# Kernel optimization log

Measured on AMD Instinct MI355X. Metric: run time of the kernel, lower is better.

## Reference

```python
import jax, jax.numpy as jnp
import numpy as np
from jax.scipy.special import logsumexp

N_ALPHA = 8192
N_BETA = 8192
N_LAYERS = 16


def setup_inputs() -> dict:
    key = jax.random.key(0)
    k1, k2, k3 = jax.random.split(key, 3)
    alpha = jax.random.uniform(k1, (N_ALPHA,), jnp.float32, 1e-3, 1.0)
    alpha = alpha / alpha.sum()
    beta = jax.random.uniform(k2, (N_BETA,), jnp.float32, 1e-3, 1.0)
    beta = beta / beta.sum()
    C = jax.random.uniform(k3, (N_ALPHA, N_BETA), jnp.float32, 0.0, 1.0)
    eps = jnp.float32(0.1)
    return {"alpha": alpha, "beta": beta, "C": C, "eps": eps}


def reference(alpha, beta, C, eps):
    # Log-domain Sinkhorn iterations (tol=None -> run all n_layers).
    log_alpha = jnp.log(alpha)
    log_beta = jnp.log(beta)

    def step(carry, _):
        _, g = carry
        # log_dot_exp(C, g, eps): logsumexp over n_beta axis of (-C + g[None,:]) / eps
        f = eps * (log_alpha - logsumexp((g[None, :] - C) / eps, axis=-1))
        # log_dot_exp(C.T, f, eps): logsumexp over n_alpha axis of (-C + f[:,None]) / eps
        g_new = eps * (log_beta - logsumexp((f[:, None] - C) / eps, axis=0))
        return (f, g_new), None

    init = (jnp.zeros_like(alpha), jnp.zeros_like(beta))
    (f, g), _ = jax.lax.scan(step, init, None, length=N_LAYERS)
    return f, g
```

## Files before the change

kernel.cpp:

```cpp
#include <hip/hip_runtime.h>

#define NA 8192
#define NB 8192
#define N_LAYERS 16
#define ROWS_PER_RC 128
#define N_RC (NA / ROWS_PER_RC)

typedef _Float16 half_t;
typedef _Float16 half4_t __attribute__((ext_vector_type(4)));
typedef _Float16 half8_t __attribute__((ext_vector_type(8)));
typedef float float4_t __attribute__((ext_vector_type(4)));

template <bool WRITE_E>
__global__ __launch_bounds__(256) void sink_u_first(
    const float* __restrict__ C, const float* __restrict__ alpha,
    const float* __restrict__ d_eps, half_t* __restrict__ E,
    float* __restrict__ u)
{
    const int row = blockIdx.x;
    const int t = threadIdx.x;
    const float inv_eps = 1.0f / d_eps[0];
    const float4_t* Crow = (const float4_t*)(C + (size_t)row * NB);
    half4_t* Erow = (half4_t*)(E + (size_t)row * NB);

    float s = 0.0f;
#pragma unroll
    for (int k = 0; k < 8; ++k) {
        const int idx = k * 256 + t;
        float4_t c = Crow[idx];
        float e0 = __expf(-c.x * inv_eps);
        float e1 = __expf(-c.y * inv_eps);
        float e2 = __expf(-c.z * inv_eps);
        float e3 = __expf(-c.w * inv_eps);
        if (WRITE_E) {
            half4_t h;
            h.x = (_Float16)e0; h.y = (_Float16)e1;
            h.z = (_Float16)e2; h.w = (_Float16)e3;
            Erow[idx] = h;
        }
        s += (e0 + e1) + (e2 + e3);
    }

    __shared__ float sm[256];
    sm[t] = s;
    __syncthreads();
    for (int off = 128; off > 0; off >>= 1) {
        if (t < off) sm[t] += sm[t + off];
        __syncthreads();
    }
    if (t == 0) u[row] = alpha[row] / sm[0];
}

template <bool USE_E>
__global__ __launch_bounds__(256) void sink_u_step(
    const void* __restrict__ mat, const float* __restrict__ v,
    const float* __restrict__ alpha, const float* __restrict__ d_eps,
    float* __restrict__ u)
{
    const int row = blockIdx.x;
    const int t = threadIdx.x;
    const float4_t* vv = (const float4_t*)v;
    float s = 0.0f;

    if (USE_E) {
        const half4_t* Erow = (const half4_t*)mat + (size_t)row * (NB / 4);
#pragma unroll
        for (int k = 0; k < 8; ++k) {
            const int idx = k * 256 + t;
            half4_t e = Erow[idx];
            float4_t w = vv[idx];
            s += (float)e.x * w.x + (float)e.y * w.y +
                 (float)e.z * w.z + (float)e.w * w.w;
        }
    } else {
        const float inv_eps = 1.0f / d_eps[0];
        const float4_t* Crow = (const float4_t*)mat + (size_t)row * (NB / 4);
#pragma unroll
        for (int k = 0; k < 8; ++k) {
            const int idx = k * 256 + t;
            float4_t c = Crow[idx];
            float4_t w = vv[idx];
            s += __expf(-c.x * inv_eps) * w.x + __expf(-c.y * inv_eps) * w.y +
                 __expf(-c.z * inv_eps) * w.z + __expf(-c.w * inv_eps) * w.w;
        }
    }

    __shared__ float sm[256];
    sm[t] = s;
    __syncthreads();
    for (int off = 128; off > 0; off >>= 1) {
        if (t < off) sm[t] += sm[t + off];
        __syncthreads();
    }
    if (t == 0) u[row] = alpha[row] / sm[0];
}

template <bool USE_E>
__global__ __launch_bounds__(256) void sink_v_partial(
    const void* __restrict__ mat, const float* __restrict__ u,
    const float* __restrict__ d_eps, float* __restrict__ partial)
{
    const int cc = blockIdx.x;
    const int rc = blockIdx.y;
    const int t = threadIdx.x;
    const int row0 = rc * ROWS_PER_RC;

    float acc[8];
#pragma unroll
    for (int k = 0; k < 8; ++k) acc[k] = 0.0f;

    if (USE_E) {
        const half8_t* Eb = (const half8_t*)mat;
        const int g = cc * 256 + t;
#pragma unroll 4
        for (int r = 0; r < ROWS_PER_RC; ++r) {
            const float ur = u[row0 + r];
            half8_t e = Eb[(size_t)(row0 + r) * (NB / 8) + g];
#pragma unroll
            for (int k = 0; k < 8; ++k) acc[k] += ur * (float)e[k];
        }
    } else {
        const float inv_eps = 1.0f / d_eps[0];
        const float4_t* Cb = (const float4_t*)mat;
        const int g = (cc * 256 + t) * 2;
#pragma unroll 2
        for (int r = 0; r < ROWS_PER_RC; ++r) {
            const float ur = u[row0 + r];
            float4_t c0 = Cb[(size_t)(row0 + r) * (NB / 4) + g];
            float4_t c1 = Cb[(size_t)(row0 + r) * (NB / 4) + g + 1];
            acc[0] += ur * __expf(-c0.x * inv_eps);
            acc[1] += ur * __expf(-c0.y * inv_eps);
            acc[2] += ur * __expf(-c0.z * inv_eps);
            acc[3] += ur * __expf(-c0.w * inv_eps);
            acc[4] += ur * __expf(-c1.x * inv_eps);
            acc[5] += ur * __expf(-c1.y * inv_eps);
            acc[6] += ur * __expf(-c1.z * inv_eps);
            acc[7] += ur * __expf(-c1.w * inv_eps);
        }
    }

    float4_t o0 = {acc[0], acc[1], acc[2], acc[3]};
    float4_t o1 = {acc[4], acc[5], acc[6], acc[7]};
    float4_t* p = (float4_t*)(partial + (size_t)rc * NB + (size_t)(cc * 256 + t) * 8);
    p[0] = o0;
    p[1] = o1;
}

__global__ __launch_bounds__(256) void sink_v_combine(
    const float* __restrict__ partial, const float* __restrict__ beta,
    float* __restrict__ v)
{
    const int col = blockIdx.x * 256 + threadIdx.x;
    float s = 0.0f;
#pragma unroll 8
    for (int rc = 0; rc < N_RC; ++rc) s += partial[(size_t)rc * NB + col];
    v[col] = beta[col] / s;
}

__global__ __launch_bounds__(256) void sink_finalize(
    const float* __restrict__ u, const float* __restrict__ v,
    const float* __restrict__ d_eps, float* __restrict__ out)
{
    const int i = blockIdx.x * 256 + threadIdx.x;
    const float eps = d_eps[0];
    if (i < NA) {
        out[i] = eps * logf(u[i]);
    } else if (i < NA + NB) {
        out[i] = eps * logf(v[i - NA]);
    }
}

extern "C" void kernel_launch(void* const* d_in, const int* in_sizes, int n_in,
                              void* d_out, int out_size, void* d_ws, size_t ws_size,
                              hipStream_t stream)
{
    const float* alpha = (const float*)d_in[0];
    const float* beta  = (const float*)d_in[1];
    const float* C     = (const float*)d_in[2];
    const float* d_eps = (const float*)d_in[3];
    float* out = (float*)d_out;

    const size_t eBytes = (size_t)NA * NB * sizeof(half_t);
    const size_t pBytes = (size_t)N_RC * NB * sizeof(float);
    const size_t vecBytes = (size_t)NA * sizeof(float);

    char* ws = (char*)d_ws;
    const bool useE = ws_size >= eBytes + pBytes + 2 * vecBytes;

    size_t off = 0;
    half_t* E = nullptr;
    if (useE) { E = (half_t*)ws; off += eBytes; }
    float* partial = (float*)(ws + off); off += pBytes;
    float* u = (float*)(ws + off); off += vecBytes;
    float* v = (float*)(ws + off); off += vecBytes;

    const dim3 blk(256);
    const dim3 gridRow(NA);
    const dim3 gridVP(NB / 2048, N_RC);
    const dim3 gridVC(NB / 256);

    for (int layer = 0; layer < N_LAYERS; ++layer) {
        if (layer == 0) {
            if (useE)
                sink_u_first<true><<<gridRow, blk, 0, stream>>>(C, alpha, d_eps, E, u);
            else
                sink_u_first<false><<<gridRow, blk, 0, stream>>>(C, alpha, d_eps, nullptr, u);
        } else {
            if (useE)
                sink_u_step<true><<<gridRow, blk, 0, stream>>>(E, v, alpha, d_eps, u);
            else
                sink_u_step<false><<<gridRow, blk, 0, stream>>>(C, v, alpha, d_eps, u);
        }
        if (useE)
            sink_v_partial<true><<<gridVP, blk, 0, stream>>>(E, u, d_eps, partial);
        else
            sink_v_partial<false><<<gridVP, blk, 0, stream>>>(C, u, d_eps, partial);
        sink_v_combine<<<gridVC, blk, 0, stream>>>(partial, beta, v);
    }
    sink_finalize<<<dim3((NA + NB) / 256), blk, 0, stream>>>(u, v, d_eps, out);
}
```

Measured before the change: 1.201 ms.

## Fuse column combine into atomic accumulation and use wave-per-row u step

Removes the separate combine kernel and the partial-sums buffer. The column partials are atomically added into a double-buffered column-sum vector, which the u-step kernel zeroes for the next layer. The u step now computes v on the fly as beta * rcp(s) and assigns one wave per row, reducing with shuffles instead of shared memory. This saves one launch per layer and the partial traffic, at the cost of 8192*128 float atomics per layer, nondeterministic summation order, and approximate reciprocals.

```diff
diff --git a/kernel.cpp b/kernel.cpp
--- a/kernel.cpp
+++ b/kernel.cpp
@@ -3,8 +3,8 @@
 #define NA 8192
 #define NB 8192
 #define N_LAYERS 16
-#define ROWS_PER_RC 128
-#define N_RC (NA / ROWS_PER_RC)
+#define ROWS_PER_VC 64
+#define N_VC (NA / ROWS_PER_VC)
 
 typedef _Float16 half_t;
 typedef _Float16 half4_t __attribute__((ext_vector_type(4)));
@@ -15,7 +15,7 @@
 __global__ __launch_bounds__(256) void sink_u_first(
     const float* __restrict__ C, const float* __restrict__ alpha,
     const float* __restrict__ d_eps, half_t* __restrict__ E,
-    float* __restrict__ u)
+    float* __restrict__ u, float* __restrict__ s_next)
 {
     const int row = blockIdx.x;
     const int t = threadIdx.x;
@@ -48,62 +48,78 @@
         if (t < off) sm[t] += sm[t + off];
         __syncthreads();
     }
-    if (t == 0) u[row] = alpha[row] / sm[0];
+    if (t == 0) {
+        u[row] = alpha[row] / sm[0];
+        s_next[row] = 0.0f;
+    }
 }
 
 template <bool USE_E>
 __global__ __launch_bounds__(256) void sink_u_step(
-    const void* __restrict__ mat, const float* __restrict__ v,
-    const float* __restrict__ alpha, const float* __restrict__ d_eps,
-    float* __restrict__ u)
-{
-    const int row = blockIdx.x;
-    const int t = threadIdx.x;
-    const float4_t* vv = (const float4_t*)v;
-    float s = 0.0f;
+    const void* __restrict__ mat, const float* __restrict__ s_prev,
+    const float* __restrict__ beta, const float* __restrict__ alpha,
+    const float* __restrict__ d_eps, float* __restrict__ u,
+    float* __restrict__ s_next)
+{
+    const int wave = threadIdx.x >> 6;
+    const int lane = threadIdx.x & 63;
+    const int row = blockIdx.x * 4 + wave;
+
+    const float4_t* bb = (const float4_t*)beta;
+    const float4_t* ss = (const float4_t*)s_prev;
+    float acc = 0.0f;
 
     if (USE_E) {
-        const half4_t* Erow = (const half4_t*)mat + (size_t)row * (NB / 4);
-#pragma unroll
-        for (int k = 0; k < 8; ++k) {
-            const int idx = k * 256 + t;
-            half4_t e = Erow[idx];
-            float4_t w = vv[idx];
-            s += (float)e.x * w.x + (float)e.y * w.y +
-                 (float)e.z * w.z + (float)e.w * w.w;
+        const half8_t* Erow = (const half8_t*)mat + (size_t)row * (NB / 8);
+#pragma unroll 4
+        for (int k = 0; k < 16; ++k) {
+            const int g = k * 64 + lane;
+            half8_t e = Erow[g];
+            float4_t b0 = bb[2 * g],     b1 = bb[2 * g + 1];
+            float4_t s0 = ss[2 * g],     s1 = ss[2 * g + 1];
+            acc += (float)e[0] * (b0.x * __builtin_amdgcn_rcpf(s0.x));
+            acc += (float)e[1] * (b0.y * __builtin_amdgcn_rcpf(s0.y));
+            acc += (float)e[2] * (b0.z * __builtin_amdgcn_rcpf(s0.z));
+            acc += (float)e[3] * (b0.w * __builtin_amdgcn_rcpf(s0.w));
+            acc += (float)e[4] * (b1.x * __builtin_amdgcn_rcpf(s1.x));
+            acc += (float)e[5] * (b1.y * __builtin_amdgcn_rcpf(s1.y));
+            acc += (float)e[6] * (b1.z * __builtin_amdgcn_rcpf(s1.z));
+            acc += (float)e[7] * (b1.w * __builtin_amdgcn_rcpf(s1.w));
         }
     } else {
         const float inv_eps = 1.0f / d_eps[0];
         const float4_t* Crow = (const float4_t*)mat + (size_t)row * (NB / 4);
-#pragma unroll
-        for (int k = 0; k < 8; ++k) {
-            const int idx = k * 256 + t;
-            float4_t c = Crow[idx];
-            float4_t w = vv[idx];
-            s += __expf(-c.x * inv_eps) * w.x + __expf(-c.y * inv_eps) * w.y +
-                 __expf(-c.z * inv_eps) * w.z + __expf(-c.w * inv_eps) * w.w;
-        }
-    }
-
-    __shared__ float sm[256];
-    sm[t] = s;
-    __syncthreads();
-    for (int off = 128; off > 0; off >>= 1) {
-        if (t < off) sm[t] += sm[t + off];
-        __syncthreads();
-    }
-    if (t == 0) u[row] = alpha[row] / sm[0];
+#pragma unroll 4
+        for (int k = 0; k < 32; ++k) {
+            const int g = k * 64 + lane;
+            float4_t c = Crow[g];
+            float4_t b = bb[g], s = ss[g];
+            acc += __expf(-c.x * inv_eps) * (b.x * __builtin_amdgcn_rcpf(s.x));
+            acc += __expf(-c.y * inv_eps) * (b.y * __builtin_amdgcn_rcpf(s.y));
+            acc += __expf(-c.z * inv_eps) * (b.z * __builtin_amdgcn_rcpf(s.z));
+            acc += __expf(-c.w * inv_eps) * (b.w * __builtin_amdgcn_rcpf(s.w));
+        }
+    }
+
+#pragma unroll
+    for (int off = 32; off > 0; off >>= 1)
+        acc += __shfl_down(acc, off, 64);
+
+    if (lane == 0) {
+        u[row] = alpha[row] / acc;
+        s_next[row] = 0.0f;
+    }
 }
 
 template <bool USE_E>
 __global__ __launch_bounds__(256) void sink_v_partial(
     const void* __restrict__ mat, const float* __restrict__ u,
-    const float* __restrict__ d_eps, float* __restrict__ partial)
+    const float* __restrict__ d_eps, float* __restrict__ s_next)
 {
     const int cc = blockIdx.x;
     const int rc = blockIdx.y;
     const int t = threadIdx.x;
-    const int row0 = rc * ROWS_PER_RC;
+    const int row0 = rc * ROWS_PER_VC;
 
     float acc[8];
 #pragma unroll
@@ -112,8 +128,8 @@
     if (USE_E) {
         const half8_t* Eb = (const half8_t*)mat;
         const int g = cc * 256 + t;
-#pragma unroll 4
-        for (int r = 0; r < ROWS_PER_RC; ++r) {
+#pragma unroll 8
+        for (int r = 0; r < ROWS_PER_VC; ++r) {
             const float ur = u[row0 + r];
             half8_t e = Eb[(size_t)(row0 + r) * (NB / 8) + g];
 #pragma unroll
@@ -123,8 +139,8 @@
         const float inv_eps = 1.0f / d_eps[0];
         const float4_t* Cb = (const float4_t*)mat;
         const int g = (cc * 256 + t) * 2;
-#pragma unroll 2
-        for (int r = 0; r < ROWS_PER_RC; ++r) {
+#pragma unroll 4
+        for (int r = 0; r < ROWS_PER_VC; ++r) {
             const float ur = u[row0 + r];
             float4_t c0 = Cb[(size_t)(row0 + r) * (NB / 4) + g];
             float4_t c1 = Cb[(size_t)(row0 + r) * (NB / 4) + g + 1];
@@ -139,34 +155,24 @@
         }
     }
 
-    float4_t o0 = {acc[0], acc[1], acc[2], acc[3]};
-    float4_t o1 = {acc[4], acc[5], acc[6], acc[7]};
-    float4_t* p = (float4_t*)(partial + (size_t)rc * NB + (size_t)(cc * 256 + t) * 8);
-    p[0] = o0;
-    p[1] = o1;
-}
-
-__global__ __launch_bounds__(256) void sink_v_combine(
-    const float* __restrict__ partial, const float* __restrict__ beta,
-    float* __restrict__ v)
-{
-    const int col = blockIdx.x * 256 + threadIdx.x;
-    float s = 0.0f;
-#pragma unroll 8
-    for (int rc = 0; rc < N_RC; ++rc) s += partial[(size_t)rc * NB + col];
-    v[col] = beta[col] / s;
+    const int col0 = (cc * 256 + t) * 8;
+#pragma unroll
+    for (int k = 0; k < 8; ++k)
+        atomicAdd(&s_next[col0 + k], acc[k]);
 }
 
 __global__ __launch_bounds__(256) void sink_finalize(
-    const float* __restrict__ u, const float* __restrict__ v,
-    const float* __restrict__ d_eps, float* __restrict__ out)
+    const float* __restrict__ u, const float* __restrict__ s_last,
+    const float* __restrict__ beta, const float* __restrict__ d_eps,
+    float* __restrict__ out)
 {
     const int i = blockIdx.x * 256 + threadIdx.x;
     const float eps = d_eps[0];
     if (i < NA) {
         out[i] = eps * logf(u[i]);
     } else if (i < NA + NB) {
-        out[i] = eps * logf(v[i - NA]);
+        const int j = i - NA;
+        out[i] = eps * logf(beta[j] / s_last[j]);
     }
 }
 
@@ -181,41 +187,43 @@
     float* out = (float*)d_out;
 
     const size_t eBytes = (size_t)NA * NB * sizeof(half_t);
-    const size_t pBytes = (size_t)N_RC * NB * sizeof(float);
     const size_t vecBytes = (size_t)NA * sizeof(float);
 
     char* ws = (char*)d_ws;
-    const bool useE = ws_size >= eBytes + pBytes + 2 * vecBytes;
+    const bool useE = ws_size >= eBytes + 3 * vecBytes;
 
     size_t off = 0;
     half_t* E = nullptr;
     if (useE) { E = (half_t*)ws; off += eBytes; }
-    float* partial = (float*)(ws + off); off += pBytes;
-    float* u = (float*)(ws + off); off += vecBytes;
-    float* v = (float*)(ws + off); off += vecBytes;
+    float* u  = (float*)(ws + off); off += vecBytes;
+    float* s0 = (float*)(ws + off); off += vecBytes;
+    float* s1 = (float*)(ws + off); off += vecBytes;
+    float* sbuf[2] = {s0, s1};
 
     const dim3 blk(256);
-    const dim3 gridRow(NA);
-    const dim3 gridVP(NB / 2048, N_RC);
-    const dim3 gridVC(NB / 256);
+    const dim3 gridFirst(NA);
+    const dim3 gridU(NA / 4);
+    const dim3 gridVP(NB / 2048, N_VC);
 
     for (int layer = 0; layer < N_LAYERS; ++layer) {
+        float* sn = sbuf[layer & 1];
         if (layer == 0) {
             if (useE)
-                sink_u_first<true><<<gridRow, blk, 0, stream>>>(C, alpha, d_eps, E, u);
+                sink_u_first<true><<<gridFirst, blk, 0, stream>>>(C, alpha, d_eps, E, u, sn);
             else
-                sink_u_first<false><<<gridRow, blk, 0, stream>>>(C, alpha, d_eps, nullptr, u);
+                sink_u_first<false><<<gridFirst, blk, 0, stream>>>(C, alpha, d_eps, nullptr, u, sn);
         } else {
+            float* sp = sbuf[(layer - 1) & 1];
             if (useE)
-                sink_u_step<true><<<gridRow, blk, 0, stream>>>(E, v, alpha, d_eps, u);
+                sink_u_step<true><<<gridU, blk, 0, stream>>>(E, sp, beta, alpha, d_eps, u, sn);
             else
-                sink_u_step<false><<<gridRow, blk, 0, stream>>>(C, v, alpha, d_eps, u);
+                sink_u_step<false><<<gridU, blk, 0, stream>>>(C, sp, beta, alpha, d_eps, u, sn);
         }
         if (useE)
-            sink_v_partial<true><<<gridVP, blk, 0, stream>>>(E, u, d_eps, partial);
+            sink_v_partial<true><<<gridVP, blk, 0, stream>>>(E, u, d_eps, sn);
         else
-            sink_v_partial<false><<<gridVP, blk, 0, stream>>>(C, u, d_eps, partial);
-        sink_v_combine<<<gridVC, blk, 0, stream>>>(partial, beta, v);
-    }
-    sink_finalize<<<dim3((NA + NB) / 256), blk, 0, stream>>>(u, v, d_eps, out);
-}
+            sink_v_partial<false><<<gridVP, blk, 0, stream>>>(C, u, d_eps, sn);
+    }
+    sink_finalize<<<dim3((NA + NB) / 256), blk, 0, stream>>>(
+        u, sbuf[(N_LAYERS - 1) & 1], beta, d_eps, out);
+}
```

New measurement: 1.710 ms. +42.4%, slower.
